# Kernel optimization log

Measured on AMD Instinct MI355X. Metric: run time of the kernel, lower is better.

The kernel has to match this reference:

```python
import jax, jax.numpy as jnp
import numpy as np

N_NODES = 100000
N_EDGES = 1600000
D_FEAT = 128
N_CLASSES = 10


def setup_inputs() -> dict:
    key = jax.random.key(0)
    ks = jax.random.split(key, 9)
    x = jax.random.normal(ks[0], (N_NODES, D_FEAT), dtype=jnp.float32)
    edge_src = jax.random.randint(ks[1], (N_EDGES,), 0, N_NODES, dtype=jnp.int32)
    edge_dst = jax.random.randint(ks[2], (N_EDGES,), 0, N_NODES, dtype=jnp.int32)
    s = 1.0 / np.sqrt(D_FEAT)
    W1 = jax.random.normal(ks[3], (D_FEAT, D_FEAT), dtype=jnp.float32) * s
    b1 = jax.random.normal(ks[4], (D_FEAT,), dtype=jnp.float32) * s
    W2 = jax.random.normal(ks[5], (D_FEAT, D_FEAT), dtype=jnp.float32) * s
    b2 = jax.random.normal(ks[6], (D_FEAT,), dtype=jnp.float32) * s
    W3 = jax.random.normal(ks[7], (D_FEAT, N_CLASSES), dtype=jnp.float32) * s
    b3 = jax.random.normal(ks[8], (N_CLASSES,), dtype=jnp.float32) * s
    return {"x": x, "edge_src": edge_src, "edge_dst": edge_dst,
            "W1": W1, "b1": b1, "W2": W2, "b2": b2, "W3": W3, "b3": b3}


def _neighbor_mean(x, src, dst, n_nodes):
    # scatter-mean of neighbor features; isolated nodes keep their own feature
    msg_sum = jax.ops.segment_sum(x[src], dst, num_segments=n_nodes)  # [N, D]
    deg = jax.ops.segment_sum(jnp.ones(src.shape, x.dtype), dst, num_segments=n_nodes)  # [N]
    mean = msg_sum / jnp.maximum(deg, 1.0)[:, None]
    return jnp.where(deg[:, None] > 0, mean, x)


def reference(x, edge_src, edge_dst, W1, b1, W2, b2, W3, b3):
    n = x.shape[0]
    # layer 1: aggregate -> linear -> tanh
    h = jnp.tanh(_neighbor_mean(x, edge_src, edge_dst, n) @ W1 + b1)
    # layer 2: aggregate -> linear -> tanh
    h = jnp.tanh(_neighbor_mean(h, edge_src, edge_dst, n) @ W2 + b2)
    # final linear head (no aggregation, no activation)
    logits = h @ W3 + b3
    return logits
```

## Files before the change

kernel.cpp:

```cpp
#include <hip/hip_runtime.h>

#define DF 128
#define AST 136
#define EPB 4096

typedef float f32x4 __attribute__((ext_vector_type(4)));
typedef short bf16x8 __attribute__((ext_vector_type(8)));

__device__ __forceinline__ ushort f2bf(float f) {
  union { float f; uint u; } c; c.f = f;
  uint u = c.u;
  uint r = (u + 0x7fffu + ((u >> 16) & 1u)) >> 16;
  return (ushort)r;
}
__device__ __forceinline__ float bf_lo(uint v) { union { uint u; float f; } c; c.u = v << 16; return c.f; }
__device__ __forceinline__ float bf_hi(uint v) { union { uint u; float f; } c; c.u = v & 0xffff0000u; return c.f; }

__device__ __forceinline__ void addv8(float* acc, uint4 v) {
  acc[0] += bf_lo(v.x); acc[1] += bf_hi(v.x);
  acc[2] += bf_lo(v.y); acc[3] += bf_hi(v.y);
  acc[4] += bf_lo(v.z); acc[5] += bf_hi(v.z);
  acc[6] += bf_lo(v.w); acc[7] += bf_hi(v.w);
}

__global__ void prep_hist_kernel(const int* __restrict__ dst, int* __restrict__ histG,
                                 int E, int nbuck, int nblocks,
                                 const float* __restrict__ x, ushort* __restrict__ xb,
                                 const float* __restrict__ W1, ushort* __restrict__ Wt1,
                                 const float* __restrict__ W2, ushort* __restrict__ Wt2,
                                 const float* __restrict__ W3, ushort* __restrict__ W3t,
                                 ushort* __restrict__ zbN, ushort* __restrict__ ybN, int n4) {
  __shared__ int lh[512];
  int tid = threadIdx.x;
  if ((int)blockIdx.x < nblocks) {
    int blk = blockIdx.x;
    for (int i = tid; i < nbuck; i += 256) lh[i] = 0;
    __syncthreads();
    int base = blk * EPB + tid * 4;
#pragma unroll
    for (int it = 0; it < EPB / 1024; ++it) {
      int e = base + it * 1024;
      if (e + 3 < E) {
        int4 d4 = *(const int4*)(dst + e);
        atomicAdd(&lh[d4.x >> 8], 1);
        atomicAdd(&lh[d4.y >> 8], 1);
        atomicAdd(&lh[d4.z >> 8], 1);
        atomicAdd(&lh[d4.w >> 8], 1);
      } else {
#pragma unroll
        for (int q = 0; q < 4; ++q) {
          int ee = e + q;
          if (ee < E) atomicAdd(&lh[dst[ee] >> 8], 1);
        }
      }
    }
    __syncthreads();
    for (int i = tid; i < nbuck; i += 256) histG[(size_t)i * nblocks + blk] = lh[i];
    return;
  }
  int i = ((int)blockIdx.x - nblocks) * 256 + tid;
  if (i < n4) {
    float4 v = ((const float4*)x)[i];
    ushort4 o; o.x = f2bf(v.x); o.y = f2bf(v.y); o.z = f2bf(v.z); o.w = f2bf(v.w);
    ((ushort4*)xb)[i] = o;
    return;
  }
  int j = i - n4;
  if (j < DF * DF) {
    int nr = j >> 7, k = j & 127;
    Wt1[j] = f2bf(W1[(size_t)k * DF + nr]);
    return;
  }
  j -= DF * DF;
  if (j < DF * DF) {
    int nr = j >> 7, k = j & 127;
    Wt2[j] = f2bf(W2[(size_t)k * DF + nr]);
    return;
  }
  j -= DF * DF;
  if (j < 16 * DF) {
    int nr = j >> 7, k = j & 127;
    W3t[j] = (nr < 10) ? f2bf(W3[(size_t)k * 10 + nr]) : (ushort)0;
    return;
  }
  j -= 16 * DF;
  if (j < 16) { ((uint4*)zbN)[j] = (uint4){0, 0, 0, 0}; return; }
  j -= 16;
  if (j < 16) { ((uint4*)ybN)[j] = (uint4){0, 0, 0, 0}; }
}

__global__ void scan1_kernel(const int* __restrict__ cnt, int* __restrict__ excl,
                             int* __restrict__ bsums, int n) {
  __shared__ int wsum[4];
  int t = threadIdx.x;
  int base = blockIdx.x * 1024 + t * 4;
  int v[4]; int s = 0;
#pragma unroll
  for (int i = 0; i < 4; i++) { int d = (base + i < n) ? cnt[base + i] : 0; v[i] = s; s += d; }
  int lane = t & 63, w = t >> 6;
  int sc = s;
#pragma unroll
  for (int off = 1; off < 64; off <<= 1) { int o = __shfl_up(sc, off); if (lane >= off) sc += o; }
  if (lane == 63) wsum[w] = sc;
  __syncthreads();
  int woff = 0;
  for (int i = 0; i < w; i++) woff += wsum[i];
  int toff = woff + (sc - s);
#pragma unroll
  for (int i = 0; i < 4; i++) if (base + i < n) excl[base + i] = toff + v[i];
  if (t == 255) bsums[blockIdx.x] = woff + sc;
}

__device__ __forceinline__ void scan_bsums_lds(const int* __restrict__ bsums, int nb,
                                               int* sbs, int* wsum) {
  int t = threadIdx.x;
  int v0 = (2 * t < nb) ? bsums[2 * t] : 0;
  int v1 = (2 * t + 1 < nb) ? bsums[2 * t + 1] : 0;
  int s = v0 + v1;
  int lane = t & 63, w = t >> 6;
  int sc = s;
#pragma unroll
  for (int off = 1; off < 64; off <<= 1) { int o = __shfl_up(sc, off); if (lane >= off) sc += o; }
  if (lane == 63) wsum[w] = sc;
  __syncthreads();
  int woff = 0;
  for (int i = 0; i < w; i++) woff += wsum[i];
  int excl = woff + sc - s;
  sbs[2 * t] = excl;
  sbs[2 * t + 1] = excl + v0;
  __syncthreads();
}

__device__ __forceinline__ void gemm_tiles(const ushort* __restrict__ A,
                                           const ushort* __restrict__ Ws,
                                           ushort* __restrict__ out, int n, int ntiles,
                                           int tile0, int tstride, int tid) {
  int lane = tid & 63, w = tid >> 6;
  int wr = (w >> 1) * 32, wc = (w & 1) * 64;
  int r16 = lane & 15, g8 = (lane >> 4) * 8;
  for (int tile = tile0; tile < ntiles; tile += tstride) {
    int node0 = tile * 64;
    int ra = node0 + wr + r16;      if (ra >= n) ra = n - 1;
    int rb = node0 + wr + 16 + r16; if (rb >= n) rb = n - 1;
    const ushort* pa = A + (size_t)ra * DF + g8;
    const ushort* pb = A + (size_t)rb * DF + g8;

    f32x4 acc[2][4];
#pragma unroll
    for (int i = 0; i < 2; i++)
#pragma unroll
      for (int j = 0; j < 4; j++) acc[i][j] = (f32x4){0.f, 0.f, 0.f, 0.f};

#pragma unroll
    for (int ks = 0; ks < 4; ++ks) {
      bf16x8 a0 = *(const bf16x8*)(pa + ks * 32);
      bf16x8 a1 = *(const bf16x8*)(pb + ks * 32);
      int k0 = ks * 32 + g8;
#pragma unroll
      for (int j = 0; j < 4; j++) {
        bf16x8 b = *(const bf16x8*)&Ws[(wc + j * 16 + r16) * AST + k0];
        acc[0][j] = __builtin_amdgcn_mfma_f32_16x16x32_bf16(a0, b, acc[0][j], 0, 0, 0);
        acc[1][j] = __builtin_amdgcn_mfma_f32_16x16x32_bf16(a1, b, acc[1][j], 0, 0, 0);
      }
    }

#pragma unroll
    for (int mi = 0; mi < 2; mi++) {
#pragma unroll
      for (int j = 0; j < 4; j++) {
        int col = wc + j * 16 + r16;
        int rowb = wr + mi * 16 + (lane >> 4) * 4;
#pragma unroll
        for (int q = 0; q < 4; q++) {
          int node = node0 + rowb + q;
          if (node < n) out[(size_t)node * DF + col] = f2bf(acc[mi][j][q]);
        }
      }
    }
  }
}

__global__ __launch_bounds__(256) void gemm_plain_kernel(
    const ushort* __restrict__ A, const ushort* __restrict__ Wt,
    ushort* __restrict__ out, int n, int ntiles) {
  __shared__ ushort Ws[128 * AST];
  int t = threadIdx.x;
  for (int i = t; i < 128 * 16; i += 256) {
    int r = i >> 4, c = i & 15;
    uint4 v = ((const uint4*)(Wt + r * DF))[c];
    *(uint4*)&Ws[r * AST + c * 8] = v;
  }
  __syncthreads();
  gemm_tiles(A, Ws, out, n, ntiles, blockIdx.x, gridDim.x, t);
}

__global__ __launch_bounds__(256) void scatter_gemm_kernel(
    const int* __restrict__ src, const int* __restrict__ dst,
    const int* __restrict__ histE, const int* __restrict__ bsums, int nb,
    uint* __restrict__ eb, int E, int nbuck, int nblocks,
    const ushort* __restrict__ xb, const ushort* __restrict__ Wt1,
    ushort* __restrict__ yb, int n, int ntiles) {
  __shared__ __align__(16) ushort Ws[128 * AST];
  int tid = threadIdx.x;
  if ((int)blockIdx.x < nblocks) {
    int* lc   = (int*)Ws;
    int* sbs  = lc + 512;
    int* wsum = sbs + 512;
    int blk = blockIdx.x;
    scan_bsums_lds(bsums, nb, sbs, wsum);
    for (int i = tid; i < nbuck; i += 256) {
      int idx = i * nblocks + blk;
      lc[i] = histE[idx] + sbs[idx >> 10];
    }
    __syncthreads();
    int base = blk * EPB + tid * 4;
#pragma unroll
    for (int it = 0; it < EPB / 1024; ++it) {
      int e = base + it * 1024;
      if (e + 3 < E) {
        int4 s4 = *(const int4*)(src + e);
        int4 d4 = *(const int4*)(dst + e);
        int p0 = atomicAdd(&lc[d4.x >> 8], 1);
        eb[p0] = (uint)s4.x | ((uint)(d4.x & 255) << 24);
        int p1 = atomicAdd(&lc[d4.y >> 8], 1);
        eb[p1] = (uint)s4.y | ((uint)(d4.y & 255) << 24);
        int p2 = atomicAdd(&lc[d4.z >> 8], 1);
        eb[p2] = (uint)s4.z | ((uint)(d4.z & 255) << 24);
        int p3 = atomicAdd(&lc[d4.w >> 8], 1);
        eb[p3] = (uint)s4.w | ((uint)(d4.w & 255) << 24);
      } else {
#pragma unroll
        for (int q = 0; q < 4; ++q) {
          int ee = e + q;
          if (ee < E) {
            int d = dst[ee];
            int pos = atomicAdd(&lc[d >> 8], 1);
            eb[pos] = (uint)src[ee] | ((uint)(d & 255) << 24);
          }
        }
      }
    }
    return;
  }
  for (int i = tid; i < 128 * 16; i += 256) {
    int r = i >> 4, c = i & 15;
    uint4 v = ((const uint4*)(Wt1 + r * DF))[c];
    *(uint4*)&Ws[r * AST + c * 8] = v;
  }
  __syncthreads();
  gemm_tiles(xb, Ws, yb, n, ntiles, (int)blockIdx.x - nblocks, (int)gridDim.x - nblocks, tid);
}

__global__ void bucket_sort_kernel(const uint* __restrict__ eb,
                                   const int* __restrict__ histE, const int* __restrict__ bsums,
                                   int nb, int* __restrict__ rowptr, int* __restrict__ csr,
                                   int N, int E, int nbuck, int nblocks) {
  __shared__ int cnt[256];
  __shared__ int cursor[256];
  __shared__ int sbs[512];
  __shared__ int wsum[4];
  int tid = threadIdx.x, b = blockIdx.x;
  scan_bsums_lds(bsums, nb, sbs, wsum);
  int idx = b * nblocks;
  int beg = histE[idx] + sbs[idx >> 10];
  int end = E;
  if (b + 1 < nbuck) { int i2 = (b + 1) * nblocks; end = histE[i2] + sbs[i2 >> 10]; }
  cnt[tid] = 0;
  __syncthreads();
  for (int e = beg + tid; e < end; e += 256)
    atomicAdd(&cnt[eb[e] >> 24], 1);
  __syncthreads();
  int v = cnt[tid];
  int lane = tid & 63, w = tid >> 6;
  int sc = v;
#pragma unroll
  for (int off = 1; off < 64; off <<= 1) { int o = __shfl_up(sc, off); if (lane >= off) sc += o; }
  if (lane == 63) wsum[w] = sc;
  __syncthreads();
  int woff = 0;
  for (int i = 0; i < w; i++) woff += wsum[i];
  int excl = woff + sc - v;
  int node = (b << 8) + tid;
  if (node <= N) rowptr[node] = beg + excl;
  cursor[tid] = beg + excl;
  __syncthreads();
  for (int e = beg + tid; e < end; e += 256) {
    uint vv = eb[e];
    int pos = atomicAdd(&cursor[vv >> 24], 1);
    csr[pos] = (int)(vv & 0x00FFFFFFu);
  }
}

__device__ __forceinline__ void gather_mean(const ushort* __restrict__ src,
                                            const int* __restrict__ rowptr,
                                            const int* __restrict__ csr,
                                            int node, int n, uint c16, float* acc) {
  int beg = rowptr[node], end = rowptr[node + 1];
  const char* xbase = (const char*)src;
#pragma unroll
  for (int i = 0; i < 8; i++) acc[i] = 0.f;
  int deg = end - beg;
  if (deg > 0) {
#pragma unroll 1
    for (int e = beg; e < end; e += 4) {
      int e1 = e + 1, e2 = e + 2, e3 = e + 3;
      uint r0 = (uint)csr[e];
      uint r1 = (e1 < end) ? (uint)csr[e1] : (uint)n;
      uint r2 = (e2 < end) ? (uint)csr[e2] : (uint)n;
      uint r3 = (e3 < end) ? (uint)csr[e3] : (uint)n;
      uint4 v0 = *(const uint4*)(xbase + (r0 * 256u + c16));
      uint4 v1 = *(const uint4*)(xbase + (r1 * 256u + c16));
      uint4 v2 = *(const uint4*)(xbase + (r2 * 256u + c16));
      uint4 v3 = *(const uint4*)(xbase + (r3 * 256u + c16));
      addv8(acc, v0);
      addv8(acc, v1);
      addv8(acc, v2);
      addv8(acc, v3);
    }
    float inv = 1.0f / (float)deg;
#pragma unroll
    for (int i = 0; i < 8; i++) acc[i] *= inv;
  } else {
    uint4 v = *(const uint4*)(xbase + ((uint)node * 256u + c16));
    float t[8] = {0, 0, 0, 0, 0, 0, 0, 0};
    addv8(t, v);
#pragma unroll
    for (int i = 0; i < 8; i++) acc[i] = t[i];
  }
}

__global__ __launch_bounds__(256) void agg_bias_tanh_kernel(
    const ushort* __restrict__ yb, const int* __restrict__ rowptr,
    const int* __restrict__ csr, const float* __restrict__ bias,
    ushort* __restrict__ h1, int n) {
  int tid = threadIdx.x;
  int node = (blockIdx.x * 256 + tid) >> 4;
  if (node >= n) return;
  uint c16 = (uint)(tid & 15) * 16u;
  float acc[8];
  gather_mean(yb, rowptr, csr, node, n, c16, acc);
  int d8 = (tid & 15) * 8;
  float4 bA = *(const float4*)(bias + d8);
  float4 bB = *(const float4*)(bias + d8 + 4);
  float h0 = tanhf(acc[0] + bA.x), hh1 = tanhf(acc[1] + bA.y);
  float h2 = tanhf(acc[2] + bA.z), h3 = tanhf(acc[3] + bA.w);
  float h4 = tanhf(acc[4] + bB.x), h5 = tanhf(acc[5] + bB.y);
  float h6 = tanhf(acc[6] + bB.z), h7 = tanhf(acc[7] + bB.w);
  uint4 r;
  r.x = (uint)f2bf(h0) | ((uint)f2bf(hh1) << 16);
  r.y = (uint)f2bf(h2) | ((uint)f2bf(h3) << 16);
  r.z = (uint)f2bf(h4) | ((uint)f2bf(h5) << 16);
  r.w = (uint)f2bf(h6) | ((uint)f2bf(h7) << 16);
  *(uint4*)((char*)h1 + ((uint)node * 256u + c16)) = r;
}

__global__ __launch_bounds__(256) void agg_head_kernel(
    const ushort* __restrict__ zb, const int* __restrict__ rowptr,
    const int* __restrict__ csr, const float* __restrict__ b2,
    const ushort* __restrict__ W3t, const float* __restrict__ b3,
    float* __restrict__ out, int n) {
  __shared__ __align__(16) ushort Hs[16 * AST];
  __shared__ __align__(16) ushort W3s[16 * AST];
  int tid = threadIdx.x;
  {
    int r = tid >> 4, c = tid & 15;
    uint4 v = ((const uint4*)(W3t + r * DF))[c];
    *(uint4*)&W3s[r * AST + c * 8] = v;
  }
  int node = (blockIdx.x * 256 + tid) >> 4;
  int node_ib = tid >> 4;
  uint c16 = (uint)(tid & 15) * 16u;
  bool active = node < n;
  uint4 hr = (uint4){0, 0, 0, 0};
  if (active) {
    float acc[8];
    gather_mean(zb, rowptr, csr, node, n, c16, acc);
    int d8 = (tid & 15) * 8;
    float4 bA = *(const float4*)(b2 + d8);
    float4 bB = *(const float4*)(b2 + d8 + 4);
    float h0 = tanhf(acc[0] + bA.x), h1 = tanhf(acc[1] + bA.y);
    float h2 = tanhf(acc[2] + bA.z), h3 = tanhf(acc[3] + bA.w);
    float h4 = tanhf(acc[4] + bB.x), h5 = tanhf(acc[5] + bB.y);
    float h6 = tanhf(acc[6] + bB.z), h7 = tanhf(acc[7] + bB.w);
    hr.x = (uint)f2bf(h0) | ((uint)f2bf(h1) << 16);
    hr.y = (uint)f2bf(h2) | ((uint)f2bf(h3) << 16);
    hr.z = (uint)f2bf(h4) | ((uint)f2bf(h5) << 16);
    hr.w = (uint)f2bf(h6) | ((uint)f2bf(h7) << 16);
  }
  *(uint4*)&Hs[node_ib * AST + (tid & 15) * 8] = hr;
  __syncthreads();

  if (tid < 64) {
    int l16 = tid & 15, g8 = (tid >> 4) * 8;
    f32x4 acc = (f32x4){0.f, 0.f, 0.f, 0.f};
#pragma unroll
    for (int ks = 0; ks < 4; ++ks) {
      bf16x8 a = *(const bf16x8*)&Hs[l16 * AST + ks * 32 + g8];
      bf16x8 b = *(const bf16x8*)&W3s[l16 * AST + ks * 32 + g8];
      acc = __builtin_amdgcn_mfma_f32_16x16x32_bf16(a, b, acc, 0, 0, 0);
    }
    if (l16 < 10) {
      float bv = b3[l16];
#pragma unroll
      for (int q = 0; q < 4; ++q) {
        int nib = (tid >> 4) * 4 + q;
        int nd = blockIdx.x * 16 + nib;
        if (nd < n) out[(size_t)nd * 10 + l16] = acc[q] + bv;
      }
    }
  }
}

extern "C" void kernel_launch(void* const* d_in, const int* in_sizes, int n_in,
                              void* d_out, int out_size, void* d_ws, size_t ws_size,
                              hipStream_t stream) {
  const float* x    = (const float*)d_in[0];
  const int*   esrc = (const int*)d_in[1];
  const int*   edst = (const int*)d_in[2];
  const float* W1   = (const float*)d_in[3];
  const float* b1   = (const float*)d_in[4];
  const float* W2   = (const float*)d_in[5];
  const float* b2   = (const float*)d_in[6];
  const float* W3   = (const float*)d_in[7];
  const float* b3   = (const float*)d_in[8];
  float* out = (float*)d_out;

  const int N = in_sizes[0] / DF;
  const int E = in_sizes[1];

  const int nbuck   = (N + 255) >> 8;
  const int nblocks = (E + EPB - 1) / EPB;
  const int M = nbuck * nblocks;

  char* ws = (char*)d_ws;
  int*  rowptr = (int*)ws;
  int*  csr    = rowptr + (N + 1);
  int*  histG  = csr + E;
  int*  histE  = histG + M;
  int*  bsums2 = histE + M;
  uint* eb     = (uint*)(bsums2 + 1024);
  size_t off = (size_t)((char*)(eb + E) - ws);
  off = (off + 255) & ~(size_t)255;
  ushort* xb  = (ushort*)(ws + off);     off += (size_t)(N + 1) * DF * 2; off = (off + 255) & ~(size_t)255;
  ushort* Wt1 = (ushort*)(ws + off);     off += (size_t)DF * DF * 2;
  ushort* Wt2 = (ushort*)(ws + off);     off += (size_t)DF * DF * 2;
  ushort* W3t = (ushort*)(ws + off);     off += (size_t)16 * DF * 2; off = (off + 255) & ~(size_t)255;
  ushort* yb  = (ushort*)(ws + off);     off += (size_t)(N + 1) * DF * 2; off = (off + 255) & ~(size_t)255;
  ushort* h1  = (ushort*)(ws + off);
  ushort* zb  = xb;

  int n4 = N * DF / 4;
  int prep_total = n4 + 2 * DF * DF + 16 * DF + 32;
  int prep_blocks = (prep_total + 255) / 256;
  prep_hist_kernel<<<nblocks + prep_blocks, 256, 0, stream>>>(
      edst, histG, E, nbuck, nblocks,
      x, xb, W1, Wt1, W2, Wt2, W3, W3t,
      xb + (size_t)N * DF, yb + (size_t)N * DF, n4);

  int nb_m = (M + 1023) / 1024;
  int ntiles = (N + 63) / 64;

  scan1_kernel<<<nb_m, 256, 0, stream>>>(histG, histE, bsums2, M);

  scatter_gemm_kernel<<<nblocks + 512, 256, 0, stream>>>(
      esrc, edst, histE, bsums2, nb_m, eb, E, nbuck, nblocks,
      xb, Wt1, yb, N, ntiles);

  bucket_sort_kernel<<<nbuck, 256, 0, stream>>>(eb, histE, bsums2, nb_m, rowptr, csr, N, E, nbuck, nblocks);

  int agg_blocks = (N + 15) / 16;

  agg_bias_tanh_kernel<<<agg_blocks, 256, 0, stream>>>(yb, rowptr, csr, b1, h1, N);
  gemm_plain_kernel<<<512, 256, 0, stream>>>(h1, Wt2, zb, N, ntiles);
  agg_head_kernel<<<agg_blocks, 256, 0, stream>>>(zb, rowptr, csr, b2, W3t, b3, out, N);
}
```

Before: 187.6 us.

## Fuse x bf16 conversion into first GEMM and fuse layer-1 aggregation with second GEMM

Removes the separate fp32-to-bf16 pass over x: the first GEMM now reads fp32 x directly and converts it in registers. The layer-1 aggregate+tanh kernel and the second GEMM kernel are merged, so each 16-node block's hidden rows go through LDS into MFMA against Wt2 and only z is written. This drops the write and re-read of the intermediate h1 and the bf16 copy of x, plus one launch. In exchange the first GEMM reads twice the bytes for x, and Wt2 is read from global/cache per block rather than staged in LDS.

Result: faster. 182.1 us (-2.9%).

```diff
diff --git a/kernel.cpp b/kernel.cpp
--- a/kernel.cpp
+++ b/kernel.cpp
@@ -23,13 +23,21 @@
   acc[6] += bf_lo(v.w); acc[7] += bf_hi(v.w);
 }
 
+__device__ __forceinline__ bf16x8 f32_to_bf16x8(const float* p) {
+  float4 a = *(const float4*)p;
+  float4 b = *(const float4*)(p + 4);
+  union { ushort u[8]; bf16x8 v; } r;
+  r.u[0] = f2bf(a.x); r.u[1] = f2bf(a.y); r.u[2] = f2bf(a.z); r.u[3] = f2bf(a.w);
+  r.u[4] = f2bf(b.x); r.u[5] = f2bf(b.y); r.u[6] = f2bf(b.z); r.u[7] = f2bf(b.w);
+  return r.v;
+}
+
 __global__ void prep_hist_kernel(const int* __restrict__ dst, int* __restrict__ histG,
                                  int E, int nbuck, int nblocks,
-                                 const float* __restrict__ x, ushort* __restrict__ xb,
                                  const float* __restrict__ W1, ushort* __restrict__ Wt1,
                                  const float* __restrict__ W2, ushort* __restrict__ Wt2,
                                  const float* __restrict__ W3, ushort* __restrict__ W3t,
-                                 ushort* __restrict__ zbN, ushort* __restrict__ ybN, int n4) {
+                                 ushort* __restrict__ zbN, ushort* __restrict__ ybN) {
   __shared__ int lh[512];
   int tid = threadIdx.x;
   if ((int)blockIdx.x < nblocks) {
@@ -58,14 +66,7 @@
     for (int i = tid; i < nbuck; i += 256) histG[(size_t)i * nblocks + blk] = lh[i];
     return;
   }
-  int i = ((int)blockIdx.x - nblocks) * 256 + tid;
-  if (i < n4) {
-    float4 v = ((const float4*)x)[i];
-    ushort4 o; o.x = f2bf(v.x); o.y = f2bf(v.y); o.z = f2bf(v.z); o.w = f2bf(v.w);
-    ((ushort4*)xb)[i] = o;
-    return;
-  }
-  int j = i - n4;
+  int j = ((int)blockIdx.x - nblocks) * 256 + tid;
   if (j < DF * DF) {
     int nr = j >> 7, k = j & 127;
     Wt1[j] = f2bf(W1[(size_t)k * DF + nr]);
@@ -131,74 +132,11 @@
   __syncthreads();
 }
 
-__device__ __forceinline__ void gemm_tiles(const ushort* __restrict__ A,
-                                           const ushort* __restrict__ Ws,
-                                           ushort* __restrict__ out, int n, int ntiles,
-                                           int tile0, int tstride, int tid) {
-  int lane = tid & 63, w = tid >> 6;
-  int wr = (w >> 1) * 32, wc = (w & 1) * 64;
-  int r16 = lane & 15, g8 = (lane >> 4) * 8;
-  for (int tile = tile0; tile < ntiles; tile += tstride) {
-    int node0 = tile * 64;
-    int ra = node0 + wr + r16;      if (ra >= n) ra = n - 1;
-    int rb = node0 + wr + 16 + r16; if (rb >= n) rb = n - 1;
-    const ushort* pa = A + (size_t)ra * DF + g8;
-    const ushort* pb = A + (size_t)rb * DF + g8;
-
-    f32x4 acc[2][4];
-#pragma unroll
-    for (int i = 0; i < 2; i++)
-#pragma unroll
-      for (int j = 0; j < 4; j++) acc[i][j] = (f32x4){0.f, 0.f, 0.f, 0.f};
-
-#pragma unroll
-    for (int ks = 0; ks < 4; ++ks) {
-      bf16x8 a0 = *(const bf16x8*)(pa + ks * 32);
-      bf16x8 a1 = *(const bf16x8*)(pb + ks * 32);
-      int k0 = ks * 32 + g8;
-#pragma unroll
-      for (int j = 0; j < 4; j++) {
-        bf16x8 b = *(const bf16x8*)&Ws[(wc + j * 16 + r16) * AST + k0];
-        acc[0][j] = __builtin_amdgcn_mfma_f32_16x16x32_bf16(a0, b, acc[0][j], 0, 0, 0);
-        acc[1][j] = __builtin_amdgcn_mfma_f32_16x16x32_bf16(a1, b, acc[1][j], 0, 0, 0);
-      }
-    }
-
-#pragma unroll
-    for (int mi = 0; mi < 2; mi++) {
-#pragma unroll
-      for (int j = 0; j < 4; j++) {
-        int col = wc + j * 16 + r16;
-        int rowb = wr + mi * 16 + (lane >> 4) * 4;
-#pragma unroll
-        for (int q = 0; q < 4; q++) {
-          int node = node0 + rowb + q;
-          if (node < n) out[(size_t)node * DF + col] = f2bf(acc[mi][j][q]);
-        }
-      }
-    }
-  }
-}
-
-__global__ __launch_bounds__(256) void gemm_plain_kernel(
-    const ushort* __restrict__ A, const ushort* __restrict__ Wt,
-    ushort* __restrict__ out, int n, int ntiles) {
-  __shared__ ushort Ws[128 * AST];
-  int t = threadIdx.x;
-  for (int i = t; i < 128 * 16; i += 256) {
-    int r = i >> 4, c = i & 15;
-    uint4 v = ((const uint4*)(Wt + r * DF))[c];
-    *(uint4*)&Ws[r * AST + c * 8] = v;
-  }
-  __syncthreads();
-  gemm_tiles(A, Ws, out, n, ntiles, blockIdx.x, gridDim.x, t);
-}
-
 __global__ __launch_bounds__(256) void scatter_gemm_kernel(
     const int* __restrict__ src, const int* __restrict__ dst,
     const int* __restrict__ histE, const int* __restrict__ bsums, int nb,
     uint* __restrict__ eb, int E, int nbuck, int nblocks,
-    const ushort* __restrict__ xb, const ushort* __restrict__ Wt1,
+    const float* __restrict__ x, const ushort* __restrict__ Wt1,
     ushort* __restrict__ yb, int n, int ntiles) {
   __shared__ __align__(16) ushort Ws[128 * AST];
   int tid = threadIdx.x;
@@ -248,7 +186,50 @@
     *(uint4*)&Ws[r * AST + c * 8] = v;
   }
   __syncthreads();
-  gemm_tiles(xb, Ws, yb, n, ntiles, (int)blockIdx.x - nblocks, (int)gridDim.x - nblocks, tid);
+
+  int lane = tid & 63, w = tid >> 6;
+  int wr = (w >> 1) * 32, wc = (w & 1) * 64;
+  int r16 = lane & 15, g8 = (lane >> 4) * 8;
+  for (int tile = (int)blockIdx.x - nblocks; tile < ntiles; tile += (int)gridDim.x - nblocks) {
+    int node0 = tile * 64;
+    int ra = node0 + wr + r16;      if (ra >= n) ra = n - 1;
+    int rb = node0 + wr + 16 + r16; if (rb >= n) rb = n - 1;
+    const float* pa = x + (size_t)ra * DF + g8;
+    const float* pb = x + (size_t)rb * DF + g8;
+
+    f32x4 acc[2][4];
+#pragma unroll
+    for (int i = 0; i < 2; i++)
+#pragma unroll
+      for (int j = 0; j < 4; j++) acc[i][j] = (f32x4){0.f, 0.f, 0.f, 0.f};
+
+#pragma unroll
+    for (int ks = 0; ks < 4; ++ks) {
+      bf16x8 a0 = f32_to_bf16x8(pa + ks * 32);
+      bf16x8 a1 = f32_to_bf16x8(pb + ks * 32);
+      int k0 = ks * 32 + g8;
+#pragma unroll
+      for (int j = 0; j < 4; j++) {
+        bf16x8 b = *(const bf16x8*)&Ws[(wc + j * 16 + r16) * AST + k0];
+        acc[0][j] = __builtin_amdgcn_mfma_f32_16x16x32_bf16(a0, b, acc[0][j], 0, 0, 0);
+        acc[1][j] = __builtin_amdgcn_mfma_f32_16x16x32_bf16(a1, b, acc[1][j], 0, 0, 0);
+      }
+    }
+
+#pragma unroll
+    for (int mi = 0; mi < 2; mi++) {
+#pragma unroll
+      for (int j = 0; j < 4; j++) {
+        int col = wc + j * 16 + r16;
+        int rowb = wr + mi * 16 + (lane >> 4) * 4;
+#pragma unroll
+        for (int q = 0; q < 4; q++) {
+          int node = node0 + rowb + q;
+          if (node < n) yb[(size_t)node * DF + col] = f2bf(acc[mi][j][q]);
+        }
+      }
+    }
+  }
 }
 
 __global__ void bucket_sort_kernel(const uint* __restrict__ eb,
@@ -329,29 +310,67 @@
   }
 }
 
-__global__ __launch_bounds__(256) void agg_bias_tanh_kernel(
+__global__ __launch_bounds__(256) void agg1_gemm_kernel(
     const ushort* __restrict__ yb, const int* __restrict__ rowptr,
-    const int* __restrict__ csr, const float* __restrict__ bias,
-    ushort* __restrict__ h1, int n) {
+    const int* __restrict__ csr, const float* __restrict__ b1,
+    const ushort* __restrict__ Wt2, ushort* __restrict__ zb, int n) {
+  __shared__ __align__(16) ushort Hs[16 * AST];
   int tid = threadIdx.x;
   int node = (blockIdx.x * 256 + tid) >> 4;
-  if (node >= n) return;
+  int node_ib = tid >> 4;
   uint c16 = (uint)(tid & 15) * 16u;
-  float acc[8];
-  gather_mean(yb, rowptr, csr, node, n, c16, acc);
-  int d8 = (tid & 15) * 8;
-  float4 bA = *(const float4*)(bias + d8);
-  float4 bB = *(const float4*)(bias + d8 + 4);
-  float h0 = tanhf(acc[0] + bA.x), hh1 = tanhf(acc[1] + bA.y);
-  float h2 = tanhf(acc[2] + bA.z), h3 = tanhf(acc[3] + bA.w);
-  float h4 = tanhf(acc[4] + bB.x), h5 = tanhf(acc[5] + bB.y);
-  float h6 = tanhf(acc[6] + bB.z), h7 = tanhf(acc[7] + bB.w);
-  uint4 r;
-  r.x = (uint)f2bf(h0) | ((uint)f2bf(hh1) << 16);
-  r.y = (uint)f2bf(h2) | ((uint)f2bf(h3) << 16);
-  r.z = (uint)f2bf(h4) | ((uint)f2bf(h5) << 16);
-  r.w = (uint)f2bf(h6) | ((uint)f2bf(h7) << 16);
-  *(uint4*)((char*)h1 + ((uint)node * 256u + c16)) = r;
+  uint4 hr = (uint4){0, 0, 0, 0};
+  if (node < n) {
+    float acc[8];
+    gather_mean(yb, rowptr, csr, node, n, c16, acc);
+    int d8 = (tid & 15) * 8;
+    float4 bA = *(const float4*)(b1 + d8);
+    float4 bB = *(const float4*)(b1 + d8 + 4);
+    float h0 = tanhf(acc[0] + bA.x), h1 = tanhf(acc[1] + bA.y);
+    float h2 = tanhf(acc[2] + bA.z), h3 = tanhf(acc[3] + bA.w);
+    float h4 = tanhf(acc[4] + bB.x), h5 = tanhf(acc[5] + bB.y);
+    float h6 = tanhf(acc[6] + bB.z), h7 = tanhf(acc[7] + bB.w);
+    hr.x = (uint)f2bf(h0) | ((uint)f2bf(h1) << 16);
+    hr.y = (uint)f2bf(h2) | ((uint)f2bf(h3) << 16);
+    hr.z = (uint)f2bf(h4) | ((uint)f2bf(h5) << 16);
+    hr.w = (uint)f2bf(h6) | ((uint)f2bf(h7) << 16);
+  }
+  *(uint4*)&Hs[node_ib * AST + (tid & 15) * 8] = hr;
+  __syncthreads();
+
+  int lane = tid & 63, w = tid >> 6;
+  int r16 = lane & 15, g8 = (lane >> 4) * 8;
+  int wc = w * 32;
+  f32x4 zacc[2];
+  zacc[0] = (f32x4){0.f, 0.f, 0.f, 0.f};
+  zacc[1] = (f32x4){0.f, 0.f, 0.f, 0.f};
+#pragma unroll
+  for (int ks = 0; ks < 4; ++ks) {
+    bf16x8 a = *(const bf16x8*)&Hs[r16 * AST + ks * 32 + g8];
+    int k0 = ks * 32 + g8;
+#pragma unroll
+    for (int j = 0; j < 2; ++j) {
+      bf16x8 b = *(const bf16x8*)&Wt2[(size_t)(wc + j * 16 + r16) * DF + k0];
+      zacc[j] = __builtin_amdgcn_mfma_f32_16x16x32_bf16(a, b, zacc[j], 0, 0, 0);
+    }
+  }
+  __syncthreads();
+
+#pragma unroll
+  for (int j = 0; j < 2; ++j) {
+    int col = wc + j * 16 + r16;
+#pragma unroll
+    for (int q = 0; q < 4; ++q) {
+      int row = (lane >> 4) * 4 + q;
+      Hs[row * AST + col] = f2bf(zacc[j][q]);
+    }
+  }
+  __syncthreads();
+
+  if (node < n) {
+    uint4 zv = *(const uint4*)&Hs[node_ib * AST + (tid & 15) * 8];
+    *(uint4*)((char*)zb + ((uint)node * 256u + c16)) = zv;
+  }
 }
 
 __global__ __launch_bounds__(256) void agg_head_kernel(
@@ -370,9 +389,8 @@
   int node = (blockIdx.x * 256 + tid) >> 4;
   int node_ib = tid >> 4;
   uint c16 = (uint)(tid & 15) * 16u;
-  bool active = node < n;
   uint4 hr = (uint4){0, 0, 0, 0};
-  if (active) {
+  if (node < n) {
     float acc[8];
     gather_mean(zb, rowptr, csr, node, n, c16, acc);
     int d8 = (tid & 15) * 8;
@@ -441,21 +459,18 @@
   uint* eb     = (uint*)(bsums2 + 1024);
   size_t off = (size_t)((char*)(eb + E) - ws);
   off = (off + 255) & ~(size_t)255;
-  ushort* xb  = (ushort*)(ws + off);     off += (size_t)(N + 1) * DF * 2; off = (off + 255) & ~(size_t)255;
   ushort* Wt1 = (ushort*)(ws + off);     off += (size_t)DF * DF * 2;
   ushort* Wt2 = (ushort*)(ws + off);     off += (size_t)DF * DF * 2;
   ushort* W3t = (ushort*)(ws + off);     off += (size_t)16 * DF * 2; off = (off + 255) & ~(size_t)255;
   ushort* yb  = (ushort*)(ws + off);     off += (size_t)(N + 1) * DF * 2; off = (off + 255) & ~(size_t)255;
-  ushort* h1  = (ushort*)(ws + off);
-  ushort* zb  = xb;
-
-  int n4 = N * DF / 4;
-  int prep_total = n4 + 2 * DF * DF + 16 * DF + 32;
+  ushort* zb  = (ushort*)(ws + off);
+
+  int prep_total = 2 * DF * DF + 16 * DF + 32;
   int prep_blocks = (prep_total + 255) / 256;
   prep_hist_kernel<<<nblocks + prep_blocks, 256, 0, stream>>>(
       edst, histG, E, nbuck, nblocks,
-      x, xb, W1, Wt1, W2, Wt2, W3, W3t,
-      xb + (size_t)N * DF, yb + (size_t)N * DF, n4);
+      W1, Wt1, W2, Wt2, W3, W3t,
+      zb + (size_t)N * DF, yb + (size_t)N * DF);
 
   int nb_m = (M + 1023) / 1024;
   int ntiles = (N + 63) / 64;
@@ -464,13 +479,12 @@
 
   scatter_gemm_kernel<<<nblocks + 512, 256, 0, stream>>>(
       esrc, edst, histE, bsums2, nb_m, eb, E, nbuck, nblocks,
-      xb, Wt1, yb, N, ntiles);
+      x, Wt1, yb, N, ntiles);
 
   bucket_sort_kernel<<<nbuck, 256, 0, stream>>>(eb, histE, bsums2, nb_m, rowptr, csr, N, E, nbuck, nblocks);
 
   int agg_blocks = (N + 15) / 16;
 
-  agg_bias_tanh_kernel<<<agg_blocks, 256, 0, stream>>>(yb, rowptr, csr, b1, h1, N);
-  gemm_plain_kernel<<<512, 256, 0, stream>>>(h1, Wt2, zb, N, ntiles);
+  agg1_gemm_kernel<<<agg_blocks, 256, 0, stream>>>(yb, rowptr, csr, b1, Wt2, zb, N);
   agg_head_kernel<<<agg_blocks, 256, 0, stream>>>(zb, rowptr, csr, b2, W3t, b3, out, N);
 }
```
